# Kernel tuning notes

Measured on AMD Instinct MI355X. Metric: run time of the kernel, lower is better.

The kernel has to match this reference:

```python
import jax, jax.numpy as jnp
import numpy as np

B, T, D = 4096, 64, 64
NE, NR = 100000, 100
PREFIXES = ["kgi", "ddp", "kgp", "ddo", "kgi1", "ddp1", "kgp1", "ddo1"]


def setup_inputs() -> dict:
    key = jax.random.key(0)
    keys = iter(jax.random.split(key, 80))
    inp = {"items": jax.random.randint(next(keys), (B,), 0, NE)}
    for p in PREFIXES:
        for s, hi in [("h0", NE), ("h1", NE), ("r0", NR), ("r1", NR), ("t0", NE), ("t1", NE)]:
            inp[p + "_" + s] = jax.random.randint(next(keys), (B, T), 0, hi)
    inp["embeddings_0"] = jax.random.normal(next(keys), (B, D), jnp.float32)
    inp["embeddings_1"] = jax.random.normal(next(keys), (B, D), jnp.float32)
    inp["entity_emb"] = jax.random.normal(next(keys), (NE, D), jnp.float32) * 0.05
    inp["relation_emb"] = jax.random.normal(next(keys), (NR, D), jnp.float32) * 0.05
    inp["W1"] = jax.random.normal(next(keys), (2 * D, D), jnp.float32) * (1.0 / np.sqrt(2 * D))
    inp["W2"] = jax.random.normal(next(keys), (D, 1), jnp.float32) * (1.0 / np.sqrt(D))
    return inp


def _knowledge_attention(h_set, path, t, W1, W2):
    # h_set, path, t: [B, T, D]; tiny sigmoid MLP -> softmax over triples -> weighted sum
    x = jnp.concatenate([h_set, path], axis=-1)                 # [B, T, 2D]
    att = jax.nn.sigmoid(jax.nn.sigmoid(x @ W1) @ W2)[..., 0]   # [B, T]
    att = jax.nn.softmax(att, axis=-1)
    return jnp.einsum('bt,btd->bd', att, t)                     # [B, D]


def _layers(E, R, W1, W2, h0, h1, r0, r1, t0, t1, init):
    # Faithful to the original n_layer=2 loop:
    #  i=0: h=E[h0], p=R[r0], t=E[t0];  i=1: h=E[h0]+E[h1], p=R[r0]*R[r1], t=E[t1]
    embs = [init]
    h, p = E[h0], R[r0]
    embs.append(_knowledge_attention(h, p, E[t0], W1, W2))
    h = h + E[h1]
    p = p * R[r1]
    embs.append(_knowledge_attention(h, p, E[t1], W1, W2))
    return embs


def reference(items, kgi_h0, kgi_h1, kgi_r0, kgi_r1, kgi_t0, kgi_t1,
              ddp_h0, ddp_h1, ddp_r0, ddp_r1, ddp_t0, ddp_t1,
              kgp_h0, kgp_h1, kgp_r0, kgp_r1, kgp_t0, kgp_t1,
              ddo_h0, ddo_h1, ddo_r0, ddo_r1, ddo_t0, ddo_t1,
              kgi1_h0, kgi1_h1, kgi1_r0, kgi1_r1, kgi1_t0, kgi1_t1,
              ddp1_h0, ddp1_h1, ddp1_r0, ddp1_r1, ddp1_t0, ddp1_t1,
              kgp1_h0, kgp1_h1, kgp1_r0, kgp1_r1, kgp1_t0, kgp1_t1,
              ddo1_h0, ddo1_h1, ddo1_r0, ddo1_r1, ddo1_t0, ddo1_t1,
              embeddings_0, embeddings_1, entity_emb, relation_emb, W1, W2):
    E, R = entity_emb, relation_emb
    kg = _layers(E, R, W1, W2, kgi_h0, kgi_h1, kgi_r0, kgi_r1, kgi_t0, kgi_t1, E[kgi_h0].mean(1))
    ddi = _layers(E, R, W1, W2, ddp_h0, ddp_h1, ddp_r0, ddp_r1, ddp_t0, ddp_t1, E[items])
    kgp = _layers(E, R, W1, W2, kgp_h0, kgp_h1, kgp_r0, kgp_r1, kgp_t0, kgp_t1, E[kgp_h0].mean(1))
    ddo = _layers(E, R, W1, W2, ddo_h0, ddo_h1, ddo_r0, ddo_r1, ddo_t0, ddo_t1, E[ddo_h0].mean(1))
    kg1 = _layers(E, R, W1, W2, kgi1_h0, kgi1_h1, kgi1_r0, kgi1_r1, kgi1_t0, kgi1_t1, E[kgi1_h0].mean(1))
    ddi1 = _layers(E, R, W1, W2, ddp1_h0, ddp1_h1, ddp1_r0, ddp1_r1, ddp1_t0, ddp1_t1, E[ddp1_h0].mean(1))
    kgp1 = _layers(E, R, W1, W2, kgp1_h0, kgp1_h1, kgp1_r0, kgp1_r1, kgp1_t0, kgp1_t1, E[kgp1_h0].mean(1))
    ddo1 = _layers(E, R, W1, W2, ddo1_h0, ddo1_h1, ddo1_r0, ddo1_r1, ddo1_t0, ddo1_t1, E[ddo1_h0].mean(1))
    del ddo, kg1, kgp1  # dead in the original score due to list aliasing/overwrite in predict()
    # predict() with agg='concat'; original aliases ddi_origin_embeddings = ddi_embeddings,
    drug_kg = [jnp.concatenate([kg[i], ddi[i]], -1) for i in range(3)]       # [B, 2D]
    drug_kg2 = [jnp.concatenate([kgp[i], ddi[i]], -1) for i in range(3)]     # [B, 2D]
    drug_d = [jnp.concatenate([ddi1[i], ddo1[i]], -1) for i in range(3)]     # [B, 2D]
    e_u = jnp.concatenate([drug_kg[2], drug_kg[1], drug_kg[0]], -1)          # [B, 6D]
    e_p_u = jnp.concatenate([drug_kg2[2], drug_kg2[1], drug_kg2[0]], -1)     # [B, 6D]
    e_i = jnp.concatenate([drug_d[2], drug_d[1], drug_d[0]], -1)             # [B, 6D]
    e1 = jnp.concatenate([e_u, e_p_u], -1)                                   # [B, 12D]
    e2 = jnp.concatenate([e_i, e_i], -1)                                     # [B, 12D] (e_p_i aliases e_i)
    scores = jax.nn.sigmoid(jnp.sum(e1 * e2, axis=-1))                       # [B]
    return scores
```

## Files before the change

### kernel.cpp

```cpp
#include <hip/hip_runtime.h>

#define BATCH 4096
#define NE 100000

typedef __attribute__((ext_vector_type(8))) short bf16x8;
typedef __attribute__((ext_vector_type(4))) float f32x4;

union U4 { uint4 u4; bf16x8 v; };

struct GPtrs {
    const int* h0[5]; const int* h1[5];
    const int* r0[5]; const int* r1[5];
    const int* t0[5]; const int* t1[5];
};

__device__ __forceinline__ unsigned trunc2(float lo, float hi){
    return __builtin_amdgcn_perm(__float_as_uint(hi), __float_as_uint(lo), 0x07060302u);
}
__device__ __forceinline__ float bflo(unsigned u){ return __uint_as_float(u << 16); }
__device__ __forceinline__ float bfhi(unsigned u){ return __uint_as_float(u & 0xFFFF0000u); }
__device__ __forceinline__ float bf2f(unsigned short h){ return __uint_as_float(((unsigned)h) << 16); }
__device__ __forceinline__ unsigned addw(unsigned x, unsigned y){
    return trunc2(bflo(x)+bflo(y), bfhi(x)+bfhi(y));
}
__device__ __forceinline__ unsigned mulw(unsigned x, unsigned y){
    return trunc2(bflo(x)*bflo(y), bfhi(x)*bfhi(y));
}
__device__ __forceinline__ float sigm(float x){ return __builtin_amdgcn_rcpf(1.0f + __expf(-x)); }

__global__ __launch_bounds__(256)
void prep_kernel(const float* __restrict__ E, const float* __restrict__ R,
                 const float* __restrict__ W1,
                 unsigned short* __restrict__ ebf, unsigned short* __restrict__ rbf,
                 uint4* __restrict__ w1pk)
{
    const int EC = (NE*64)/8;
    const int RC = (100*64)/8;
    const int WC = 1024;
    int stride = gridDim.x * blockDim.x;
    for (int c = blockIdx.x*blockDim.x + threadIdx.x; c < EC + RC + WC; c += stride) {
        if (c < EC + RC) {
            const float* src; unsigned short* dst;
            if (c < EC) { src = E + c*8;      dst = ebf + c*8; }
            else        { src = R + (c-EC)*8; dst = rbf + (c-EC)*8; }
            float4 a = *(const float4*)src;
            float4 b = *(const float4*)(src + 4);
            uint4 o;
            o.x = trunc2(a.x,a.y); o.y = trunc2(a.z,a.w);
            o.z = trunc2(b.x,b.y); o.w = trunc2(b.z,b.w);
            *(uint4*)dst = o;
        } else {
            int c2   = c - (EC + RC);
            int frag = c2 >> 6;
            int ln   = c2 & 63;
            int row  = (frag >> 2)*16 + (ln & 15);
            int kp0  = (frag & 3)*16 + 4*(ln >> 4);
            uint4 o;
            o.x = trunc2(W1[(2*kp0    )*64 + row], W1[(2*kp0 + 1)*64 + row]);
            o.y = trunc2(W1[(2*kp0 + 2)*64 + row], W1[(2*kp0 + 3)*64 + row]);
            o.z = trunc2(W1[(2*kp0 + 4)*64 + row], W1[(2*kp0 + 5)*64 + row]);
            o.w = trunc2(W1[(2*kp0 + 6)*64 + row], W1[(2*kp0 + 7)*64 + row]);
            w1pk[c2] = o;
        }
    }
}

__global__ __launch_bounds__(256, 2)
void group_kernel(GPtrs gp, const int* __restrict__ items,
                  const float* __restrict__ E,
                  const unsigned short* __restrict__ ebf,
                  const unsigned short* __restrict__ rbf,
                  const uint4* __restrict__ w1pk, const float* __restrict__ W2,
                  float* __restrict__ ws)
{
    const int g    = blockIdx.y;
    const int b0   = blockIdx.x*2;
    const int b1   = b0 + 1;
    const int tid  = threadIdx.x;
    const int lane = tid & 63;
    const int wv   = tid >> 6;

    __shared__ uint4 wlds[1024];
    __shared__ float red_log[2][2][64];
    __shared__ float red_pv[2][2][4][64];

    wlds[tid      ] = w1pk[tid      ];
    wlds[tid + 256] = w1pk[tid + 256];
    wlds[tid + 512] = w1pk[tid + 512];
    wlds[tid + 768] = w1pk[tid + 768];

    const int tcol = lane & 15;
    const int q    = lane >> 4;
    const int q4   = q * 4;
    const int t_   = wv*16 + tcol;

    int vh0A = gp.h0[g][b0*64 + lane], vh0B = gp.h0[g][b1*64 + lane];
    int vh1A = gp.h1[g][b0*64 + lane], vh1B = gp.h1[g][b1*64 + lane];
    int vr0A = gp.r0[g][b0*64 + lane], vr0B = gp.r0[g][b1*64 + lane];
    int vr1A = gp.r1[g][b0*64 + lane], vr1B = gp.r1[g][b1*64 + lane];
    int vt0A = gp.t0[g][b0*64 + lane], vt0B = gp.t0[g][b1*64 + lane];
    int vt1A = gp.t1[g][b0*64 + lane], vt1B = gp.t1[g][b1*64 + lane];

    __syncthreads();

    if (g == 1) {
        if (wv == 0) ws[((g*3 + 0)*BATCH + b0)*64 + lane] = E[items[b0]*64 + lane];
        if (wv == 1) ws[((g*3 + 0)*BATCH + b1)*64 + lane] = E[items[b1]*64 + lane];
    } else {
        float a0 = 0.f, a1 = 0.f, a2 = 0.f, a3 = 0.f;
        float c0 = 0.f, c1 = 0.f, c2 = 0.f, c3 = 0.f;
        #pragma unroll
        for (int u = 0; u < 16; u += 4) {
            int t = wv*16 + u;
            int rA0 = __shfl(vh0A, t,   64), rB0 = __shfl(vh0B, t,   64);
            int rA1 = __shfl(vh0A, t+1, 64), rB1 = __shfl(vh0B, t+1, 64);
            int rA2 = __shfl(vh0A, t+2, 64), rB2 = __shfl(vh0B, t+2, 64);
            int rA3 = __shfl(vh0A, t+3, 64), rB3 = __shfl(vh0B, t+3, 64);
            a0 += bf2f(ebf[rA0*64 + lane]); c0 += bf2f(ebf[rB0*64 + lane]);
            a1 += bf2f(ebf[rA1*64 + lane]); c1 += bf2f(ebf[rB1*64 + lane]);
            a2 += bf2f(ebf[rA2*64 + lane]); c2 += bf2f(ebf[rB2*64 + lane]);
            a3 += bf2f(ebf[rA3*64 + lane]); c3 += bf2f(ebf[rB3*64 + lane]);
        }
        red_pv[0][0][wv][lane] = (a0+a1)+(a2+a3);
        red_pv[0][1][wv][lane] = (c0+c1)+(c2+c3);
        __syncthreads();
        if (wv < 2) {
            int bb = (wv == 0) ? b0 : b1;
            ws[((g*3 + 0)*BATCH + bb)*64 + lane] =
                (red_pv[0][wv][0][lane]+red_pv[0][wv][1][lane]+
                 red_pv[0][wv][2][lane]+red_pv[0][wv][3][lane]) * (1.0f/64.0f);
        }
    }

    U4 fA0, fA1, fA2, fA3, fB0, fB1, fB2, fB3;
    {
        int hrA = __shfl(vh0A, t_, 64), hrB = __shfl(vh0B, t_, 64);
        int prA = __shfl(vr0A, t_, 64), prB = __shfl(vr0B, t_, 64);
        const uint4* hpA = (const uint4*)(ebf + hrA*64);
        const uint4* hpB = (const uint4*)(ebf + hrB*64);
        const uint4* ppA = (const uint4*)(rbf + prA*64);
        const uint4* ppB = (const uint4*)(rbf + prB*64);
        fA0.u4 = hpA[q];     fB0.u4 = hpB[q];
        fA1.u4 = hpA[4 + q]; fB1.u4 = hpB[4 + q];
        fA2.u4 = ppA[q];     fB2.u4 = ppB[q];
        fA3.u4 = ppA[4 + q]; fB3.u4 = ppB[4 + q];
    }

    #pragma unroll
    for (int L = 0; L < 2; ++L) {
        if (L == 1) {
            int hrA = __shfl(vh1A, t_, 64), hrB = __shfl(vh1B, t_, 64);
            int prA = __shfl(vr1A, t_, 64), prB = __shfl(vr1B, t_, 64);
            const uint4* hqA = (const uint4*)(ebf + hrA*64);
            const uint4* hqB = (const uint4*)(ebf + hrB*64);
            const uint4* pqA = (const uint4*)(rbf + prA*64);
            const uint4* pqB = (const uint4*)(rbf + prB*64);
            uint4 xA0 = hqA[q], xA1 = hqA[4+q], yA0 = pqA[q], yA1 = pqA[4+q];
            uint4 xB0 = hqB[q], xB1 = hqB[4+q], yB0 = pqB[q], yB1 = pqB[4+q];
            fA0.u4 = make_uint4(addw(fA0.u4.x,xA0.x), addw(fA0.u4.y,xA0.y),
                                addw(fA0.u4.z,xA0.z), addw(fA0.u4.w,xA0.w));
            fB0.u4 = make_uint4(addw(fB0.u4.x,xB0.x), addw(fB0.u4.y,xB0.y),
                                addw(fB0.u4.z,xB0.z), addw(fB0.u4.w,xB0.w));
            fA1.u4 = make_uint4(addw(fA1.u4.x,xA1.x), addw(fA1.u4.y,xA1.y),
                                addw(fA1.u4.z,xA1.z), addw(fA1.u4.w,xA1.w));
            fB1.u4 = make_uint4(addw(fB1.u4.x,xB1.x), addw(fB1.u4.y,xB1.y),
                                addw(fB1.u4.z,xB1.z), addw(fB1.u4.w,xB1.w));
            fA2.u4 = make_uint4(mulw(fA2.u4.x,yA0.x), mulw(fA2.u4.y,yA0.y),
                                mulw(fA2.u4.z,yA0.z), mulw(fA2.u4.w,yA0.w));
            fB2.u4 = make_uint4(mulw(fB2.u4.x,yB0.x), mulw(fB2.u4.y,yB0.y),
                                mulw(fB2.u4.z,yB0.z), mulw(fB2.u4.w,yB0.w));
            fA3.u4 = make_uint4(mulw(fA3.u4.x,yA1.x), mulw(fA3.u4.y,yA1.y),
                                mulw(fA3.u4.z,yA1.z), mulw(fA3.u4.w,yA1.w));
            fB3.u4 = make_uint4(mulw(fB3.u4.x,yB1.x), mulw(fB3.u4.y,yB1.y),
                                mulw(fB3.u4.z,yB1.z), mulw(fB3.u4.w,yB1.w));
        }

        float ptA = 0.f, ptB = 0.f;
        #pragma unroll
        for (int jt = 0; jt < 4; ++jt) {
            U4 wf0, wf1, wf2, wf3;
            wf0.u4 = wlds[(jt*4 + 0)*64 + lane];
            wf1.u4 = wlds[(jt*4 + 1)*64 + lane];
            wf2.u4 = wlds[(jt*4 + 2)*64 + lane];
            wf3.u4 = wlds[(jt*4 + 3)*64 + lane];
            f32x4 accA = {0.f, 0.f, 0.f, 0.f};
            f32x4 accB = {0.f, 0.f, 0.f, 0.f};
            accA = __builtin_amdgcn_mfma_f32_16x16x32_bf16(wf0.v, fA0.v, accA, 0,0,0);
            accB = __builtin_amdgcn_mfma_f32_16x16x32_bf16(wf0.v, fB0.v, accB, 0,0,0);
            accA = __builtin_amdgcn_mfma_f32_16x16x32_bf16(wf1.v, fA1.v, accA, 0,0,0);
            accB = __builtin_amdgcn_mfma_f32_16x16x32_bf16(wf1.v, fB1.v, accB, 0,0,0);
            accA = __builtin_amdgcn_mfma_f32_16x16x32_bf16(wf2.v, fA2.v, accA, 0,0,0);
            accB = __builtin_amdgcn_mfma_f32_16x16x32_bf16(wf2.v, fB2.v, accB, 0,0,0);
            accA = __builtin_amdgcn_mfma_f32_16x16x32_bf16(wf3.v, fA3.v, accA, 0,0,0);
            accB = __builtin_amdgcn_mfma_f32_16x16x32_bf16(wf3.v, fB3.v, accB, 0,0,0);
            float4 w2v = *(const float4*)(W2 + jt*16 + q4);
            ptA += sigm(accA[0])*w2v.x + sigm(accA[1])*w2v.y
                 + sigm(accA[2])*w2v.z + sigm(accA[3])*w2v.w;
            ptB += sigm(accB[0])*w2v.x + sigm(accB[1])*w2v.y
                 + sigm(accB[2])*w2v.z + sigm(accB[3])*w2v.w;
        }
        ptA += __shfl_xor(ptA, 16, 64); ptB += __shfl_xor(ptB, 16, 64);
        ptA += __shfl_xor(ptA, 32, 64); ptB += __shfl_xor(ptB, 32, 64);
        if (lane < 16) {
            red_log[L][0][wv*16 + lane] = sigm(ptA);
            red_log[L][1][wv*16 + lane] = sigm(ptB);
        }
        __syncthreads();

        float eA = __expf(red_log[L][0][lane]);
        float eB = __expf(red_log[L][1][lane]);
        float dA = eA, dB = eB;
        #pragma unroll
        for (int m = 32; m > 0; m >>= 1) {
            dA += __shfl_xor(dA, m, 64);
            dB += __shfl_xor(dB, m, 64);
        }
        float attA = eA * __builtin_amdgcn_rcpf(dA);
        float attB = eB * __builtin_amdgcn_rcpf(dB);

        int vtA = (L == 0) ? vt0A : vt1A;
        int vtB = (L == 0) ? vt0B : vt1B;
        float oA0 = 0.f, oA1 = 0.f, oA2 = 0.f, oA3 = 0.f;
        float oB0 = 0.f, oB1 = 0.f, oB2 = 0.f, oB3 = 0.f;
        #pragma unroll
        for (int u = 0; u < 16; u += 4) {
            int t = wv*16 + u;
            int rA0 = __shfl(vtA, t,   64), rB0 = __shfl(vtB, t,   64);
            int rA1 = __shfl(vtA, t+1, 64), rB1 = __shfl(vtB, t+1, 64);
            int rA2 = __shfl(vtA, t+2, 64), rB2 = __shfl(vtB, t+2, 64);
            int rA3 = __shfl(vtA, t+3, 64), rB3 = __shfl(vtB, t+3, 64);
            float aA0 = __shfl(attA, t,   64), aB0 = __shfl(attB, t,   64);
            float aA1 = __shfl(attA, t+1, 64), aB1 = __shfl(attB, t+1, 64);
            float aA2 = __shfl(attA, t+2, 64), aB2 = __shfl(attB, t+2, 64);
            float aA3 = __shfl(attA, t+3, 64), aB3 = __shfl(attB, t+3, 64);
            oA0 = fmaf(aA0, bf2f(ebf[rA0*64 + lane]), oA0);
            oB0 = fmaf(aB0, bf2f(ebf[rB0*64 + lane]), oB0);
            oA1 = fmaf(aA1, bf2f(ebf[rA1*64 + lane]), oA1);
            oB1 = fmaf(aB1, bf2f(ebf[rB1*64 + lane]), oB1);
            oA2 = fmaf(aA2, bf2f(ebf[rA2*64 + lane]), oA2);
            oB2 = fmaf(aB2, bf2f(ebf[rB2*64 + lane]), oB2);
            oA3 = fmaf(aA3, bf2f(ebf[rA3*64 + lane]), oA3);
            oB3 = fmaf(aB3, bf2f(ebf[rB3*64 + lane]), oB3);
        }
        red_pv[L][0][wv][lane] = (oA0+oA1)+(oA2+oA3);
        red_pv[L][1][wv][lane] = (oB0+oB1)+(oB2+oB3);
        __syncthreads();
        if (wv < 2) {
            int bb = (wv == 0) ? b0 : b1;
            ws[((g*3 + 1 + L)*BATCH + bb)*64 + lane] =
                red_pv[L][wv][0][lane]+red_pv[L][wv][1][lane]+
                red_pv[L][wv][2][lane]+red_pv[L][wv][3][lane];
        }
    }
}

__launch_bounds__(256, 4)
__global__ void combine_kernel(const float* __restrict__ ws, float* __restrict__ out)
{
    const int tid  = threadIdx.x;
    const int lane = tid & 63;
    const int wv   = tid >> 6;
    const int b    = blockIdx.x*4 + wv;
    float acc = 0.f;
    #pragma unroll
    for (int i = 0; i < 3; ++i) {
        float kg   = ws[((0*3+i)*BATCH + b)*64 + lane];
        float ddi  = ws[((1*3+i)*BATCH + b)*64 + lane];
        float kgp  = ws[((2*3+i)*BATCH + b)*64 + lane];
        float ddi1 = ws[((3*3+i)*BATCH + b)*64 + lane];
        float ddo1 = ws[((4*3+i)*BATCH + b)*64 + lane];
        acc += (kg + kgp)*ddi1 + 2.0f*ddi*ddo1;
    }
    #pragma unroll
    for (int m = 32; m > 0; m >>= 1) acc += __shfl_xor(acc, m, 64);
    if (lane == 0) out[b] = 1.0f/(1.0f + __expf(-acc));
}

extern "C" void kernel_launch(void* const* d_in, const int* in_sizes, int n_in,
                              void* d_out, int out_size, void* d_ws, size_t ws_size,
                              hipStream_t stream)
{
    const int gbase[5] = {1, 7, 13, 31, 43};
    GPtrs gp;
    for (int g = 0; g < 5; ++g) {
        gp.h0[g] = (const int*)d_in[gbase[g]+0];
        gp.h1[g] = (const int*)d_in[gbase[g]+1];
        gp.r0[g] = (const int*)d_in[gbase[g]+2];
        gp.r1[g] = (const int*)d_in[gbase[g]+3];
        gp.t0[g] = (const int*)d_in[gbase[g]+4];
        gp.t1[g] = (const int*)d_in[gbase[g]+5];
    }
    const int*   items = (const int*)d_in[0];
    const float* E     = (const float*)d_in[51];
    const float* R     = (const float*)d_in[52];
    const float* W1    = (const float*)d_in[53];
    const float* W2    = (const float*)d_in[54];

    float*          ws  = (float*)d_ws;
    unsigned short* ebf = (unsigned short*)((char*)d_ws + 15728640);
    unsigned short* rbf = (unsigned short*)((char*)d_ws + 15728640 + 12800000);
    uint4*          w1pk= (uint4*)((char*)d_ws + 15728640 + 12800000 + 12800 + 64);

    prep_kernel<<<1024, 256, 0, stream>>>(E, R, W1, ebf, rbf, w1pk);
    dim3 grid(BATCH/2, 5);
    group_kernel<<<grid, 256, 0, stream>>>(gp, items, E, ebf, rbf, w1pk, W2, ws);
    combine_kernel<<<BATCH/4, 256, 0, stream>>>(ws, (float*)d_out);
}
```

Measured before the change: 165.6 us.

## Gather embedding rows as 32-bit pairs and fold log2e into W1

The h-mean and attention-weighted t-sum gathers now load two bf16 values per lane as one 32-bit word. Each wave covers two triples per iteration, which halves the number of gather load instructions and shuffles, with a cross-half shuffle reduction at the end. W1 is pre-scaled by log2(e) during prep so the first sigmoid can use exp2 directly and skip a multiply. The pre-scaling changes bf16 rounding of W1 slightly, and the gather loops add extra shuffle-xor steps.

New measurement: 160.9 us. 1.03x faster.

```diff
diff --git a/kernel.cpp b/kernel.cpp
--- a/kernel.cpp
+++ b/kernel.cpp
@@ -2,6 +2,7 @@
 
 #define BATCH 4096
 #define NE 100000
+#define LOG2E 1.44269504088896f
 
 typedef __attribute__((ext_vector_type(8))) short bf16x8;
 typedef __attribute__((ext_vector_type(4))) float f32x4;
@@ -19,7 +20,6 @@
 }
 __device__ __forceinline__ float bflo(unsigned u){ return __uint_as_float(u << 16); }
 __device__ __forceinline__ float bfhi(unsigned u){ return __uint_as_float(u & 0xFFFF0000u); }
-__device__ __forceinline__ float bf2f(unsigned short h){ return __uint_as_float(((unsigned)h) << 16); }
 __device__ __forceinline__ unsigned addw(unsigned x, unsigned y){
     return trunc2(bflo(x)+bflo(y), bfhi(x)+bfhi(y));
 }
@@ -27,6 +27,9 @@
     return trunc2(bflo(x)*bflo(y), bfhi(x)*bfhi(y));
 }
 __device__ __forceinline__ float sigm(float x){ return __builtin_amdgcn_rcpf(1.0f + __expf(-x)); }
+__device__ __forceinline__ float sigm2(float y){
+    return __builtin_amdgcn_rcpf(1.0f + exp2f(-y));
+}
 
 __global__ __launch_bounds__(256)
 void prep_kernel(const float* __restrict__ E, const float* __restrict__ R,
@@ -56,10 +59,10 @@
             int row  = (frag >> 2)*16 + (ln & 15);
             int kp0  = (frag & 3)*16 + 4*(ln >> 4);
             uint4 o;
-            o.x = trunc2(W1[(2*kp0    )*64 + row], W1[(2*kp0 + 1)*64 + row]);
-            o.y = trunc2(W1[(2*kp0 + 2)*64 + row], W1[(2*kp0 + 3)*64 + row]);
-            o.z = trunc2(W1[(2*kp0 + 4)*64 + row], W1[(2*kp0 + 5)*64 + row]);
-            o.w = trunc2(W1[(2*kp0 + 6)*64 + row], W1[(2*kp0 + 7)*64 + row]);
+            o.x = trunc2(W1[(2*kp0    )*64 + row]*LOG2E, W1[(2*kp0 + 1)*64 + row]*LOG2E);
+            o.y = trunc2(W1[(2*kp0 + 2)*64 + row]*LOG2E, W1[(2*kp0 + 3)*64 + row]*LOG2E);
+            o.z = trunc2(W1[(2*kp0 + 4)*64 + row]*LOG2E, W1[(2*kp0 + 5)*64 + row]*LOG2E);
+            o.w = trunc2(W1[(2*kp0 + 6)*64 + row]*LOG2E, W1[(2*kp0 + 7)*64 + row]*LOG2E);
             w1pk[c2] = o;
         }
     }
@@ -93,6 +96,9 @@
     const int q    = lane >> 4;
     const int q4   = q * 4;
     const int t_   = wv*16 + tcol;
+    const int bt   = wv*16 + (lane>>5);
+    const int col  = lane & 31;
+    const unsigned* e32 = (const unsigned*)ebf;
 
     int vh0A = gp.h0[g][b0*64 + lane], vh0B = gp.h0[g][b1*64 + lane];
     int vh1A = gp.h1[g][b0*64 + lane], vh1B = gp.h1[g][b1*64 + lane];
@@ -107,22 +113,25 @@
         if (wv == 0) ws[((g*3 + 0)*BATCH + b0)*64 + lane] = E[items[b0]*64 + lane];
         if (wv == 1) ws[((g*3 + 0)*BATCH + b1)*64 + lane] = E[items[b1]*64 + lane];
     } else {
-        float a0 = 0.f, a1 = 0.f, a2 = 0.f, a3 = 0.f;
-        float c0 = 0.f, c1 = 0.f, c2 = 0.f, c3 = 0.f;
+        float aL0=0.f,aH0=0.f,aL1=0.f,aH1=0.f;
+        float cL0=0.f,cH0=0.f,cL1=0.f,cH1=0.f;
         #pragma unroll
-        for (int u = 0; u < 16; u += 4) {
-            int t = wv*16 + u;
-            int rA0 = __shfl(vh0A, t,   64), rB0 = __shfl(vh0B, t,   64);
-            int rA1 = __shfl(vh0A, t+1, 64), rB1 = __shfl(vh0B, t+1, 64);
-            int rA2 = __shfl(vh0A, t+2, 64), rB2 = __shfl(vh0B, t+2, 64);
-            int rA3 = __shfl(vh0A, t+3, 64), rB3 = __shfl(vh0B, t+3, 64);
-            a0 += bf2f(ebf[rA0*64 + lane]); c0 += bf2f(ebf[rB0*64 + lane]);
-            a1 += bf2f(ebf[rA1*64 + lane]); c1 += bf2f(ebf[rB1*64 + lane]);
-            a2 += bf2f(ebf[rA2*64 + lane]); c2 += bf2f(ebf[rB2*64 + lane]);
-            a3 += bf2f(ebf[rA3*64 + lane]); c3 += bf2f(ebf[rB3*64 + lane]);
-        }
-        red_pv[0][0][wv][lane] = (a0+a1)+(a2+a3);
-        red_pv[0][1][wv][lane] = (c0+c1)+(c2+c3);
+        for (int u = 0; u < 8; ++u) {
+            int tt = bt + 2*u;
+            int rA = __shfl(vh0A, tt, 64);
+            int rB = __shfl(vh0B, tt, 64);
+            unsigned wa = e32[rA*32 + col];
+            unsigned wb = e32[rB*32 + col];
+            if (u & 1) { aL1 += bflo(wa); aH1 += bfhi(wa); cL1 += bflo(wb); cH1 += bfhi(wb); }
+            else       { aL0 += bflo(wa); aH0 += bfhi(wa); cL0 += bflo(wb); cH0 += bfhi(wb); }
+        }
+        float aL = aL0+aL1, aH = aH0+aH1, cL = cL0+cL1, cH = cH0+cH1;
+        aL += __shfl_xor(aL, 32, 64); aH += __shfl_xor(aH, 32, 64);
+        cL += __shfl_xor(cL, 32, 64); cH += __shfl_xor(cH, 32, 64);
+        if (lane < 32) {
+            ((float2*)red_pv[0][0][wv])[lane] = make_float2(aL, aH);
+            ((float2*)red_pv[0][1][wv])[lane] = make_float2(cL, cH);
+        }
         __syncthreads();
         if (wv < 2) {
             int bb = (wv == 0) ? b0 : b1;
@@ -194,10 +203,10 @@
             accA = __builtin_amdgcn_mfma_f32_16x16x32_bf16(wf3.v, fA3.v, accA, 0,0,0);
             accB = __builtin_amdgcn_mfma_f32_16x16x32_bf16(wf3.v, fB3.v, accB, 0,0,0);
             float4 w2v = *(const float4*)(W2 + jt*16 + q4);
-            ptA += sigm(accA[0])*w2v.x + sigm(accA[1])*w2v.y
-                 + sigm(accA[2])*w2v.z + sigm(accA[3])*w2v.w;
-            ptB += sigm(accB[0])*w2v.x + sigm(accB[1])*w2v.y
-                 + sigm(accB[2])*w2v.z + sigm(accB[3])*w2v.w;
+            ptA += sigm2(accA[0])*w2v.x + sigm2(accA[1])*w2v.y
+                 + sigm2(accA[2])*w2v.z + sigm2(accA[3])*w2v.w;
+            ptB += sigm2(accB[0])*w2v.x + sigm2(accB[1])*w2v.y
+                 + sigm2(accB[2])*w2v.z + sigm2(accB[3])*w2v.w;
         }
         ptA += __shfl_xor(ptA, 16, 64); ptB += __shfl_xor(ptB, 16, 64);
         ptA += __shfl_xor(ptA, 32, 64); ptB += __shfl_xor(ptB, 32, 64);
@@ -220,30 +229,32 @@
 
         int vtA = (L == 0) ? vt0A : vt1A;
         int vtB = (L == 0) ? vt0B : vt1B;
-        float oA0 = 0.f, oA1 = 0.f, oA2 = 0.f, oA3 = 0.f;
-        float oB0 = 0.f, oB1 = 0.f, oB2 = 0.f, oB3 = 0.f;
+        float aL0=0.f,aH0=0.f,aL1=0.f,aH1=0.f;
+        float cL0=0.f,cH0=0.f,cL1=0.f,cH1=0.f;
         #pragma unroll
-        for (int u = 0; u < 16; u += 4) {
-            int t = wv*16 + u;
-            int rA0 = __shfl(vtA, t,   64), rB0 = __shfl(vtB, t,   64);
-            int rA1 = __shfl(vtA, t+1, 64), rB1 = __shfl(vtB, t+1, 64);
-            int rA2 = __shfl(vtA, t+2, 64), rB2 = __shfl(vtB, t+2, 64);
-            int rA3 = __shfl(vtA, t+3, 64), rB3 = __shfl(vtB, t+3, 64);
-            float aA0 = __shfl(attA, t,   64), aB0 = __shfl(attB, t,   64);
-            float aA1 = __shfl(attA, t+1, 64), aB1 = __shfl(attB, t+1, 64);
-            float aA2 = __shfl(attA, t+2, 64), aB2 = __shfl(attB, t+2, 64);
-            float aA3 = __shfl(attA, t+3, 64), aB3 = __shfl(attB, t+3, 64);
-            oA0 = fmaf(aA0, bf2f(ebf[rA0*64 + lane]), oA0);
-            oB0 = fmaf(aB0, bf2f(ebf[rB0*64 + lane]), oB0);
-            oA1 = fmaf(aA1, bf2f(ebf[rA1*64 + lane]), oA1);
-            oB1 = fmaf(aB1, bf2f(ebf[rB1*64 + lane]), oB1);
-            oA2 = fmaf(aA2, bf2f(ebf[rA2*64 + lane]), oA2);
-            oB2 = fmaf(aB2, bf2f(ebf[rB2*64 + lane]), oB2);
-            oA3 = fmaf(aA3, bf2f(ebf[rA3*64 + lane]), oA3);
-            oB3 = fmaf(aB3, bf2f(ebf[rB3*64 + lane]), oB3);
-        }
-        red_pv[L][0][wv][lane] = (oA0+oA1)+(oA2+oA3);
-        red_pv[L][1][wv][lane] = (oB0+oB1)+(oB2+oB3);
+        for (int u = 0; u < 8; ++u) {
+            int tt = bt + 2*u;
+            int rA = __shfl(vtA, tt, 64);
+            float wA = __shfl(attA, tt, 64);
+            int rB = __shfl(vtB, tt, 64);
+            float wB = __shfl(attB, tt, 64);
+            unsigned da = e32[rA*32 + col];
+            unsigned db = e32[rB*32 + col];
+            if (u & 1) {
+                aL1 = fmaf(wA, bflo(da), aL1); aH1 = fmaf(wA, bfhi(da), aH1);
+                cL1 = fmaf(wB, bflo(db), cL1); cH1 = fmaf(wB, bfhi(db), cH1);
+            } else {
+                aL0 = fmaf(wA, bflo(da), aL0); aH0 = fmaf(wA, bfhi(da), aH0);
+                cL0 = fmaf(wB, bflo(db), cL0); cH0 = fmaf(wB, bfhi(db), cH0);
+            }
+        }
+        float aL = aL0+aL1, aH = aH0+aH1, cL = cL0+cL1, cH = cH0+cH1;
+        aL += __shfl_xor(aL, 32, 64); aH += __shfl_xor(aH, 32, 64);
+        cL += __shfl_xor(cL, 32, 64); cH += __shfl_xor(cH, 32, 64);
+        if (lane < 32) {
+            ((float2*)red_pv[L][0][wv])[lane] = make_float2(aL, aH);
+            ((float2*)red_pv[L][1][wv])[lane] = make_float2(cL, cH);
+        }
         __syncthreads();
         if (wv < 2) {
             int bb = (wv == 0) ? b0 : b1;
```
